# Optimization experiments

Hardware: AMD Instinct MI355X
Metric: run time of the kernel (lower is better)

Reference implementation:

```python
import jax, jax.numpy as jnp
import numpy as np

W_HARD = 0.5
W_SOFT = 0.5
IGNORE_INDEX = -100
TEMPERATURE = 1.0


def setup_inputs() -> dict:
    key = jax.random.key(0)
    k1, k2, k3, k4, k5 = jax.random.split(key, 5)
    BT, HS, HT, V = 2048, 2048, 4096, 32000
    return {
        "student_input": jax.random.normal(k1, (BT, HS), jnp.float32) * 0.02,
        "student_weight": jax.random.normal(k2, (V, HS), jnp.float32) * 0.02,
        "teacher_input": jax.random.normal(k3, (BT, HT), jnp.float32) * 0.02,
        "teacher_weight": jax.random.normal(k4, (V, HT), jnp.float32) * 0.02,
        "true_labels": jax.random.randint(k5, (BT,), 0, V, jnp.int32),
    }


def reference(student_input, student_weight, teacher_input, teacher_weight, true_labels):
    # Fused linear + JSD distillation loss (Liger semantics).
    BT = student_input.shape[0]
    s_logits = student_input @ student_weight.T  # (BT, V)
    t_logits = teacher_input @ teacher_weight.T  # (BT, V)

    # Hard loss: cross entropy on student logits, sum over non-ignored, / BT
    logp = jax.nn.log_softmax(s_logits, axis=-1)
    valid = true_labels != IGNORE_INDEX
    safe_labels = jnp.where(valid, true_labels, 0)
    nll = -jnp.take_along_axis(logp, safe_labels[:, None], axis=-1)[:, 0]
    hard_loss = jnp.sum(jnp.where(valid, nll, 0.0)) / BT

    # Soft loss: JSD between temperature-softened student/teacher distributions,
    # batchmean over all BT tokens.
    s_lp = jax.nn.log_softmax(s_logits / TEMPERATURE, axis=-1)
    t_lp = jax.nn.log_softmax(t_logits / TEMPERATURE, axis=-1)
    s_p = jnp.exp(s_lp)
    t_p = jnp.exp(t_lp)
    log_m = jnp.log((s_p + t_p) * 0.5)
    student_kl = jnp.sum(s_p * (s_lp - log_m)) / BT
    teacher_kl = jnp.sum(t_p * (t_lp - log_m)) / BT
    soft_loss = (student_kl + teacher_kl) * 0.5

    return W_HARD * hard_loss + W_SOFT * soft_loss
```

## Files before the change

### kernel.cpp

```cpp
#include <hip/hip_runtime.h>
#include <hip/hip_bf16.h>
#include <cstdint>
#include <cstddef>

#define BT 2048
#define V  32000
#define HS 2048
#define HT 4096

typedef float f32x4 __attribute__((ext_vector_type(4)));
typedef __bf16 bf16x8 __attribute__((ext_vector_type(8)));
typedef unsigned short u16x8 __attribute__((ext_vector_type(8)));

__device__ __forceinline__ unsigned short f2bf(float f) {
    union { float f; unsigned u; } x; x.f = f;
    unsigned u = x.u;
    unsigned r = (u + 0x7FFFu + ((u >> 16) & 1u)) >> 16;
    return (unsigned short)r;
}

__device__ __forceinline__ void gload_lds16(const void* g, void* l) {
    __builtin_amdgcn_global_load_lds(
        (__attribute__((address_space(1))) void*)(void*)g,
        (__attribute__((address_space(3))) void*)l, 16, 0, 0);
}

__global__ __launch_bounds__(256)
void convert_bf16(const float* __restrict__ in, unsigned short* __restrict__ out,
                  int n8) {
    int i = blockIdx.x * 256 + threadIdx.x;
    if (i >= n8) return;
    const float4* p = (const float4*)in + (size_t)i * 2;
    float4 a = p[0], b = p[1];
    u16x8 r;
    r[0] = f2bf(a.x); r[1] = f2bf(a.y); r[2] = f2bf(a.z); r[3] = f2bf(a.w);
    r[4] = f2bf(b.x); r[5] = f2bf(b.y); r[6] = f2bf(b.z); r[7] = f2bf(b.w);
    ((u16x8*)out)[i] = r;
}

template <int K>
__global__ __launch_bounds__(256, 2)
void gemm_bf16(const unsigned short* __restrict__ A,
               const unsigned short* __restrict__ W,
               float* __restrict__ C) {
    __shared__ __align__(16) unsigned short As[128 * 32];
    __shared__ __align__(16) unsigned short Bs[128 * 32];

    const int tid  = threadIdx.x;
    const int m0   = blockIdx.x * 128;
    const int n0   = blockIdx.y * 128;
    const int wave = tid >> 6;
    const int lane = tid & 63;
    const int ln15 = lane & 15;
    const int q    = lane >> 4;
    const int wr   = wave >> 1;
    const int wc   = wave & 1;

    const int sr = tid >> 2;
    const int cs = tid & 3;
    const int cg = cs ^ (sr & 3);

    const unsigned short* ga0 = A + (size_t)(m0 + sr) * K + cg * 8;
    const unsigned short* ga1 = ga0 + (size_t)64 * K;
    const unsigned short* gb0 = W + (size_t)(n0 + sr) * K + cg * 8;
    const unsigned short* gb1 = gb0 + (size_t)64 * K;
    unsigned short* la0 = &As[sr * 32 + cs * 8];
    unsigned short* la1 = la0 + 64 * 32;
    unsigned short* lb0 = &Bs[sr * 32 + cs * 8];
    unsigned short* lb1 = lb0 + 64 * 32;

    f32x4 acc[4][4];
#pragma unroll
    for (int i = 0; i < 4; ++i)
#pragma unroll
        for (int j = 0; j < 4; ++j)
            acc[i][j] = f32x4{0.f, 0.f, 0.f, 0.f};

    const int sl = q ^ (ln15 & 3);

    for (int k0 = 0; k0 < K; k0 += 32) {
        gload_lds16(ga0 + k0, la0);
        gload_lds16(ga1 + k0, la1);
        gload_lds16(gb0 + k0, lb0);
        gload_lds16(gb1 + k0, lb1);
        __syncthreads();

        bf16x8 af[4], bfv[4];
#pragma unroll
        for (int t = 0; t < 4; ++t) {
            af[t]  = *(const bf16x8*)&As[(wr * 64 + t * 16 + ln15) * 32 + sl * 8];
            bfv[t] = *(const bf16x8*)&Bs[(wc * 64 + t * 16 + ln15) * 32 + sl * 8];
        }
#pragma unroll
        for (int i = 0; i < 4; ++i)
#pragma unroll
            for (int j = 0; j < 4; ++j)
                acc[i][j] = __builtin_amdgcn_mfma_f32_16x16x32_bf16(
                    af[i], bfv[j], acc[i][j], 0, 0, 0);
        __syncthreads();
    }

#pragma unroll
    for (int i = 0; i < 4; ++i) {
        const int row = m0 + wr * 64 + i * 16 + q * 4;
#pragma unroll
        for (int j = 0; j < 4; ++j) {
            const int col = n0 + wc * 64 + j * 16 + ln15;
#pragma unroll
            for (int r = 0; r < 4; ++r)
                C[(size_t)(row + r) * V + col] = acc[i][j][r];
        }
    }
}

template <int K>
__global__ __launch_bounds__(256, 2)
void gemm_f32(const float* __restrict__ A, const float* __restrict__ W,
              float* __restrict__ C) {
    __shared__ __align__(16) unsigned short As[128][40];
    __shared__ __align__(16) unsigned short Bs[128][40];

    const int tid  = threadIdx.x;
    const int m0   = blockIdx.x * 128;
    const int n0   = blockIdx.y * 128;
    const int wave = tid >> 6;
    const int lane = tid & 63;
    const int ln15 = lane & 15;
    const int q    = lane >> 4;
    const int wr   = wave >> 1;
    const int wc   = wave & 1;

    f32x4 acc[4][4];
#pragma unroll
    for (int i = 0; i < 4; ++i)
#pragma unroll
        for (int j = 0; j < 4; ++j)
            acc[i][j] = f32x4{0.f, 0.f, 0.f, 0.f};

    const int lr = tid >> 3;
    const int lc = (tid & 7) * 4;

    for (int k0 = 0; k0 < K; k0 += 32) {
#pragma unroll
        for (int p = 0; p < 4; ++p) {
            const int r = lr + p * 32;
            const float4 av = *(const float4*)&A[(size_t)(m0 + r) * K + k0 + lc];
            const float4 bv = *(const float4*)&W[(size_t)(n0 + r) * K + k0 + lc];
            As[r][lc + 0] = f2bf(av.x); As[r][lc + 1] = f2bf(av.y);
            As[r][lc + 2] = f2bf(av.z); As[r][lc + 3] = f2bf(av.w);
            Bs[r][lc + 0] = f2bf(bv.x); Bs[r][lc + 1] = f2bf(bv.y);
            Bs[r][lc + 2] = f2bf(bv.z); Bs[r][lc + 3] = f2bf(bv.w);
        }
        __syncthreads();

        bf16x8 af[4], bfr[4];
#pragma unroll
        for (int t = 0; t < 4; ++t) {
            af[t]  = *(const bf16x8*)&As[wr * 64 + t * 16 + ln15][q * 8];
            bfr[t] = *(const bf16x8*)&Bs[wc * 64 + t * 16 + ln15][q * 8];
        }
#pragma unroll
        for (int i = 0; i < 4; ++i)
#pragma unroll
            for (int j = 0; j < 4; ++j)
                acc[i][j] = __builtin_amdgcn_mfma_f32_16x16x32_bf16(
                    af[i], bfr[j], acc[i][j], 0, 0, 0);
        __syncthreads();
    }

#pragma unroll
    for (int i = 0; i < 4; ++i) {
        const int row = m0 + wr * 64 + i * 16 + q * 4;
#pragma unroll
        for (int j = 0; j < 4; ++j) {
            const int col = n0 + wc * 64 + j * 16 + ln15;
#pragma unroll
            for (int r = 0; r < 4; ++r)
                C[(size_t)(row + r) * V + col] = acc[i][j][r];
        }
    }
}

__device__ __forceinline__ void ol_update(float& m, float& s, float x) {
    float M = fmaxf(m, x);
    s = s * __expf(m - M) + __expf(x - M);
    m = M;
}

__global__ __launch_bounds__(256)
void stats_loss(const float* __restrict__ S, const float* __restrict__ T,
                const int* __restrict__ labels, float* __restrict__ out) {
    const int row = blockIdx.x;
    const int tid = threadIdx.x;
    const float4* s4 = (const float4*)(S + (size_t)row * V);
    const float4* t4 = (const float4*)(T + (size_t)row * V);
    const int NV4 = V / 4;

    float ms = -1e30f, ss = 0.f, mt = -1e30f, st = 0.f;
    for (int i = tid; i < NV4; i += 256) {
        float4 a = s4[i];
        ol_update(ms, ss, a.x); ol_update(ms, ss, a.y);
        ol_update(ms, ss, a.z); ol_update(ms, ss, a.w);
        float4 b = t4[i];
        ol_update(mt, st, b.x); ol_update(mt, st, b.y);
        ol_update(mt, st, b.z); ol_update(mt, st, b.w);
    }

    __shared__ float rm[256], rs[256];
    rm[tid] = ms; rs[tid] = ss; __syncthreads();
    for (int off = 128; off > 0; off >>= 1) {
        if (tid < off) {
            float m1 = rm[tid], s1 = rs[tid];
            float m2 = rm[tid + off], s2 = rs[tid + off];
            float M = fmaxf(m1, m2);
            rm[tid] = M;
            rs[tid] = s1 * __expf(m1 - M) + s2 * __expf(m2 - M);
        }
        __syncthreads();
    }
    const float lseS = rm[0] + __logf(rs[0]);
    __syncthreads();
    rm[tid] = mt; rs[tid] = st; __syncthreads();
    for (int off = 128; off > 0; off >>= 1) {
        if (tid < off) {
            float m1 = rm[tid], s1 = rs[tid];
            float m2 = rm[tid + off], s2 = rs[tid + off];
            float M = fmaxf(m1, m2);
            rm[tid] = M;
            rs[tid] = s1 * __expf(m1 - M) + s2 * __expf(m2 - M);
        }
        __syncthreads();
    }
    const float lseT = rm[0] + __logf(rs[0]);
    __syncthreads();

    float acc = 0.f;
    for (int i = tid; i < NV4; i += 256) {
        float4 a = s4[i];
        float4 b = t4[i];
#pragma unroll
        for (int c = 0; c < 4; ++c) {
            float ls = ((const float*)&a)[c] - lseS;
            float lt = ((const float*)&b)[c] - lseT;
            float ps = __expf(ls);
            float pt = __expf(lt);
            float lm = __logf(0.5f * (ps + pt));
            acc += ps * (ls - lm) + pt * (lt - lm);
        }
    }
    rm[tid] = acc; __syncthreads();
    for (int off = 128; off > 0; off >>= 1) {
        if (tid < off) rm[tid] += rm[tid + off];
        __syncthreads();
    }
    if (tid == 0) {
        const int lab = labels[row];
        float nll = 0.f;
        if (lab != -100) nll = lseS - S[(size_t)row * V + lab];
        const float contrib = (0.5f * nll + 0.25f * rm[0]) * (1.0f / (float)BT);
        atomicAdd(out, contrib);
    }
}

__global__ void zero_out(float* out) { out[0] = 0.f; }

extern "C" void kernel_launch(void* const* d_in, const int* in_sizes, int n_in,
                              void* d_out, int out_size, void* d_ws, size_t ws_size,
                              hipStream_t stream) {
    const float* s_in   = (const float*)d_in[0];
    const float* s_w    = (const float*)d_in[1];
    const float* t_in   = (const float*)d_in[2];
    const float* t_w    = (const float*)d_in[3];
    const int*   labels = (const int*)d_in[4];
    float* out = (float*)d_out;

    char* ws = (char*)d_ws;
    const size_t logit_bytes = (size_t)BT * V * sizeof(float);
    float* s_logits = (float*)ws;
    float* t_logits = (float*)(ws + logit_bytes);
    size_t off = 2 * logit_bytes;

    const size_t as_bytes = (size_t)BT * HS * 2;
    const size_t ws_bytes = (size_t)V  * HS * 2;
    const size_t at_bytes = (size_t)BT * HT * 2;
    const size_t wt_bytes = (size_t)V  * HT * 2;
    const size_t fast_total = off + as_bytes + ws_bytes + at_bytes + wt_bytes + 4096;

    zero_out<<<1, 1, 0, stream>>>(out);

    if (ws_size >= fast_total) {
        unsigned short* abf_s = (unsigned short*)(ws + off);  off += as_bytes;
        unsigned short* wbf_s = (unsigned short*)(ws + off);  off += ws_bytes;
        unsigned short* abf_t = (unsigned short*)(ws + off);  off += at_bytes;
        unsigned short* wbf_t = (unsigned short*)(ws + off);  off += wt_bytes;

        const int n8_as = BT * HS / 8, n8_ws = V * HS / 8;
        const int n8_at = BT * HT / 8, n8_wt = V * HT / 8;
        convert_bf16<<<(n8_as + 255) / 256, 256, 0, stream>>>(s_in, abf_s, n8_as);
        convert_bf16<<<(n8_ws + 255) / 256, 256, 0, stream>>>(s_w,  wbf_s, n8_ws);
        convert_bf16<<<(n8_at + 255) / 256, 256, 0, stream>>>(t_in, abf_t, n8_at);
        convert_bf16<<<(n8_wt + 255) / 256, 256, 0, stream>>>(t_w,  wbf_t, n8_wt);

        gemm_bf16<HS><<<dim3(BT / 128, V / 128), 256, 0, stream>>>(abf_s, wbf_s, s_logits);
        gemm_bf16<HT><<<dim3(BT / 128, V / 128), 256, 0, stream>>>(abf_t, wbf_t, t_logits);
    } else {
        gemm_f32<HS><<<dim3(BT / 128, V / 128), 256, 0, stream>>>(s_in, s_w, s_logits);
        gemm_f32<HT><<<dim3(BT / 128, V / 128), 256, 0, stream>>>(t_in, t_w, t_logits);
    }

    stats_loss<<<BT, 256, 0, stream>>>(s_logits, t_logits, labels, out);
}
```

Measured before the change: 2.081 ms.

## Replace bf16 GEMM with 256x256 double-buffered pipelined MFMA kernel

Replaces the 128x128 single-buffered bf16 GEMM with a 256x256 tile, 512-thread kernel that uses a K-step of 64 and double-buffered LDS. Global-to-LDS loads are interleaved with MFMA phases using explicit vmcnt/lgkmcnt waits, barriers and s_setprio. It also adds a workgroup-index swizzle for L2 locality and an 8-way XOR LDS swizzle. The goals are to overlap memory with compute, raise arithmetic intensity per tile and cut barrier stalls. The costs are 128KB of LDS per block, heavy register use for 32 accumulators, and a hand-scheduled pipeline that is fragile to get right.

```diff
diff --git a/kernel.cpp b/kernel.cpp
--- a/kernel.cpp
+++ b/kernel.cpp
@@ -39,78 +39,134 @@
 }
 
 template <int K>
-__global__ __launch_bounds__(256, 2)
-void gemm_bf16(const unsigned short* __restrict__ A,
-               const unsigned short* __restrict__ W,
-               float* __restrict__ C) {
-    __shared__ __align__(16) unsigned short As[128 * 32];
-    __shared__ __align__(16) unsigned short Bs[128 * 32];
-
-    const int tid  = threadIdx.x;
-    const int m0   = blockIdx.x * 128;
-    const int n0   = blockIdx.y * 128;
-    const int wave = tid >> 6;
-    const int lane = tid & 63;
-    const int ln15 = lane & 15;
-    const int q    = lane >> 4;
-    const int wr   = wave >> 1;
-    const int wc   = wave & 1;
-
-    const int sr = tid >> 2;
-    const int cs = tid & 3;
-    const int cg = cs ^ (sr & 3);
-
-    const unsigned short* ga0 = A + (size_t)(m0 + sr) * K + cg * 8;
-    const unsigned short* ga1 = ga0 + (size_t)64 * K;
-    const unsigned short* gb0 = W + (size_t)(n0 + sr) * K + cg * 8;
-    const unsigned short* gb1 = gb0 + (size_t)64 * K;
-    unsigned short* la0 = &As[sr * 32 + cs * 8];
-    unsigned short* la1 = la0 + 64 * 32;
-    unsigned short* lb0 = &Bs[sr * 32 + cs * 8];
-    unsigned short* lb1 = lb0 + 64 * 32;
-
-    f32x4 acc[4][4];
-#pragma unroll
-    for (int i = 0; i < 4; ++i)
+__global__ __launch_bounds__(512, 2)
+void gemm_bf16_256(const unsigned short* __restrict__ A,
+                   const unsigned short* __restrict__ W,
+                   float* __restrict__ C) {
+    __shared__ __align__(16) unsigned short As[2][256 * 64];
+    __shared__ __align__(16) unsigned short Bs[2][256 * 64];
+
+    const int tid = threadIdx.x;
+
+    constexpr int GX = BT / 256;
+    constexpr int PERX = (BT / 256) * (V / 256) / 8;
+    const int wg  = blockIdx.y * GX + blockIdx.x;
+    const int swz = (wg & 7) * PERX + (wg >> 3);
+    const int m0 = (swz & 7) * 256;
+    const int n0 = (swz >> 3) * 256;
+
+    const int wave = tid >> 6, lane = tid & 63;
+    const int ln15 = lane & 15, qlane = lane >> 4;
+    const int wr = wave >> 2;
+    const int wc = wave & 3;
+
+    const int trow = tid >> 3;
+    const int cs8  = tid & 7;
+    const int gch  = cs8 ^ (trow & 7);
+    const int arow = trow + (tid >= 256 ? 96 : 0);
+
+    const unsigned short* pA = A + (size_t)(m0 + arow) * K + gch * 8;
+    const unsigned short* pB = W + (size_t)(n0 + trow) * K + gch * 8;
+    const int aoff = arow * 64 + cs8 * 8;
+    const int boff = trow * 64 + cs8 * 8;
+
+#define SA(kt, b, j) gload_lds16(pA + (size_t)(j) * 32 * K + (size_t)(kt) * 64, \
+                                 &As[b][(j) * 2048 + aoff])
+#define SB(kt, b, j) gload_lds16(pB + (size_t)(j) * 64 * K + (size_t)(kt) * 64, \
+                                 &Bs[b][(j) * 4096 + boff])
+#define BAR() __builtin_amdgcn_s_barrier()
+#define VM6() asm volatile("s_waitcnt vmcnt(6)" ::: "memory")
+#define VM0() asm volatile("s_waitcnt vmcnt(0)" ::: "memory")
+#define LGKM0() do { asm volatile("s_waitcnt lgkmcnt(0)" ::: "memory"); \
+                     __builtin_amdgcn_sched_barrier(0); } while (0)
+
+    const int sl0 = ((qlane)     ^ (ln15 & 7)) * 8;
+    const int sl1 = ((qlane ^ 4) ^ (ln15 & 7)) * 8;
+    const int abase = (wr * 128 + ln15) * 64;
+    const int bbase = (wc * 64  + ln15) * 64;
+
+    f32x4 acc[8][4];
+#pragma unroll
+    for (int i = 0; i < 8; ++i)
 #pragma unroll
         for (int j = 0; j < 4; ++j)
             acc[i][j] = f32x4{0.f, 0.f, 0.f, 0.f};
 
-    const int sl = q ^ (ln15 & 3);
-
-    for (int k0 = 0; k0 < K; k0 += 32) {
-        gload_lds16(ga0 + k0, la0);
-        gload_lds16(ga1 + k0, la1);
-        gload_lds16(gb0 + k0, lb0);
-        gload_lds16(gb1 + k0, lb1);
-        __syncthreads();
-
-        bf16x8 af[4], bfv[4];
-#pragma unroll
-        for (int t = 0; t < 4; ++t) {
-            af[t]  = *(const bf16x8*)&As[(wr * 64 + t * 16 + ln15) * 32 + sl * 8];
-            bfv[t] = *(const bf16x8*)&Bs[(wc * 64 + t * 16 + ln15) * 32 + sl * 8];
-        }
-#pragma unroll
-        for (int i = 0; i < 4; ++i)
-#pragma unroll
-            for (int j = 0; j < 4; ++j)
-                acc[i][j] = __builtin_amdgcn_mfma_f32_16x16x32_bf16(
-                    af[i], bfv[j], acc[i][j], 0, 0, 0);
-        __syncthreads();
-    }
-
-#pragma unroll
-    for (int i = 0; i < 4; ++i) {
-        const int row = m0 + wr * 64 + i * 16 + q * 4;
-#pragma unroll
-        for (int j = 0; j < 4; ++j) {
-            const int col = n0 + wc * 64 + j * 16 + ln15;
+    bf16x8 bfv[4][2];
+    bf16x8 af[2][2];
+
+#define LOADB(b) do { _Pragma("unroll") for (int cb = 0; cb < 4; ++cb) {      \
+        bfv[cb][0] = *(const bf16x8*)&Bs[b][bbase + cb * 1024 + sl0];         \
+        bfv[cb][1] = *(const bf16x8*)&Bs[b][bbase + cb * 1024 + sl1]; } } while (0)
+#define LOADA(b, q) do { _Pragma("unroll") for (int i = 0; i < 2; ++i) {      \
+        af[i][0] = *(const bf16x8*)&As[b][abase + ((q) * 2 + i) * 1024 + sl0];\
+        af[i][1] = *(const bf16x8*)&As[b][abase + ((q) * 2 + i) * 1024 + sl1]; } } while (0)
+#define MM(q) do { __builtin_amdgcn_s_setprio(1);                             \
+        _Pragma("unroll") for (int ks = 0; ks < 2; ++ks)                      \
+        _Pragma("unroll") for (int i = 0; i < 2; ++i)                         \
+        _Pragma("unroll") for (int cb = 0; cb < 4; ++cb)                      \
+            acc[(q) * 2 + i][cb] = __builtin_amdgcn_mfma_f32_16x16x32_bf16(   \
+                af[i][ks], bfv[cb][ks], acc[(q) * 2 + i][cb], 0, 0, 0);       \
+        __builtin_amdgcn_s_setprio(0); } while (0)
+
+    SB(0, 0, 0); SB(0, 0, 1); SB(0, 0, 2); SB(0, 0, 3);
+    SA(0, 0, 0); SA(0, 0, 1); SA(0, 0, 2); SA(0, 0, 3);
+    SB(1, 1, 0); SB(1, 1, 1); SB(1, 1, 2); SB(1, 1, 3);
+    SA(1, 1, 0); SA(1, 1, 1);
+    VM6();
+    BAR();
+
+    constexpr int NT = K / 64;
+    constexpr int NI = NT / 2;
+    for (int i = 0; i < NI - 1; ++i) {
+        const int t2 = 2 * i + 2, t3 = 2 * i + 3;
+        LOADB(0); LOADA(0, 0); SA(2 * i + 1, 1, 2); SA(2 * i + 1, 1, 3);
+        BAR(); LGKM0(); MM(0); BAR();
+        LOADA(0, 1); SB(t2, 0, 0); SB(t2, 0, 1);
+        BAR(); LGKM0(); MM(1); BAR();
+        LOADA(0, 2); SB(t2, 0, 2); SB(t2, 0, 3);
+        BAR(); LGKM0(); MM(2); BAR();
+        LOADA(0, 3); SA(t2, 0, 0); SA(t2, 0, 1);
+        BAR(); LGKM0(); MM(3); VM6(); BAR();
+        LOADB(1); LOADA(1, 0); SA(t2, 0, 2); SA(t2, 0, 3);
+        BAR(); LGKM0(); MM(0); BAR();
+        LOADA(1, 1); SB(t3, 1, 0); SB(t3, 1, 1);
+        BAR(); LGKM0(); MM(1); BAR();
+        LOADA(1, 2); SB(t3, 1, 2); SB(t3, 1, 3);
+        BAR(); LGKM0(); MM(2); BAR();
+        LOADA(1, 3); SA(t3, 1, 0); SA(t3, 1, 1);
+        BAR(); LGKM0(); MM(3); VM6(); BAR();
+    }
+    LOADB(0); LOADA(0, 0); SA(NT - 1, 1, 2); SA(NT - 1, 1, 3);
+    BAR(); LGKM0(); MM(0); BAR();
+    LOADA(0, 1); BAR(); LGKM0(); MM(1); BAR();
+    LOADA(0, 2); BAR(); LGKM0(); MM(2); BAR();
+    LOADA(0, 3); BAR(); LGKM0(); MM(3); VM0(); BAR();
+    LOADB(1); LOADA(1, 0); BAR(); LGKM0(); MM(0); BAR();
+    LOADA(1, 1); BAR(); LGKM0(); MM(1); BAR();
+    LOADA(1, 2); BAR(); LGKM0(); MM(2); BAR();
+    LOADA(1, 3); LGKM0(); MM(3);
+
+#pragma unroll
+    for (int rb = 0; rb < 8; ++rb) {
+        const int row = m0 + wr * 128 + rb * 16 + qlane * 4;
+#pragma unroll
+        for (int cb = 0; cb < 4; ++cb) {
+            const int col = n0 + wc * 64 + cb * 16 + ln15;
 #pragma unroll
             for (int r = 0; r < 4; ++r)
-                C[(size_t)(row + r) * V + col] = acc[i][j][r];
-        }
-    }
+                C[(size_t)(row + r) * V + col] = acc[rb][cb][r];
+        }
+    }
+#undef SA
+#undef SB
+#undef BAR
+#undef VM6
+#undef VM0
+#undef LGKM0
+#undef LOADB
+#undef LOADA
+#undef MM
 }
 
 template <int K>
@@ -301,8 +357,8 @@
         convert_bf16<<<(n8_at + 255) / 256, 256, 0, stream>>>(t_in, abf_t, n8_at);
         convert_bf16<<<(n8_wt + 255) / 256, 256, 0, stream>>>(t_w,  wbf_t, n8_wt);
 
-        gemm_bf16<HS><<<dim3(BT / 128, V / 128), 256, 0, stream>>>(abf_s, wbf_s, s_logits);
-        gemm_bf16<HT><<<dim3(BT / 128, V / 128), 256, 0, stream>>>(abf_t, wbf_t, t_logits);
+        gemm_bf16_256<HS><<<dim3(BT / 256, V / 256), 512, 0, stream>>>(abf_s, wbf_s, s_logits);
+        gemm_bf16_256<HT><<<dim3(BT / 256, V / 256), 512, 0, stream>>>(abf_t, wbf_t, t_logits);
     } else {
         gemm_f32<HS><<<dim3(BT / 128, V / 128), 256, 0, stream>>>(s_in, s_w, s_logits);
         gemm_f32<HT><<<dim3(BT / 128, V / 128), 256, 0, stream>>>(t_in, t_w, t_logits);
```

Measured after the change: 1.889 ms. 9.2% less time.
